# Kernel optimization log

Measured on AMD Instinct MI355X. Metric: run time of the kernel, lower is better.

## Reference

```python
import jax, jax.numpy as jnp
import numpy as np

VOCAB, FDIM = 100000, 256
N_NODES, N_UNIQUE, NUM_SAMPLE = 4096, 16384, 10
NEG = -9.0e15


def setup_inputs() -> dict:
    key = jax.random.key(0)
    k0, k1, k2, k3 = jax.random.split(key, 4)
    features = jax.random.normal(k0, (VOCAB, FDIM), dtype=jnp.float32)
    nodes = jax.random.randint(k1, (N_NODES,), 0, VOCAB, dtype=jnp.int64 if jax.config.jax_enable_x64 else jnp.int32)
    unique_ids = jax.random.randint(k2, (N_UNIQUE,), 0, VOCAB, dtype=nodes.dtype)
    neigh_idx = jax.random.randint(k3, (N_NODES, NUM_SAMPLE), 0, N_UNIQUE, dtype=nodes.dtype)
    return {"features": features, "nodes": nodes, "unique_ids": unique_ids, "neigh_idx": neigh_idx}


def reference(features, nodes, unique_ids, neigh_idx):
    # features: [V, F] lookup table (the `features` callable of the module)
    # nodes: [N] batch node ids; unique_ids: [M] unique sampled-neighbor ids
    # neigh_idx: [N, S] columns (into unique_ids) of each node's sampled neighbors
    N, _ = neigh_idx.shape
    M = unique_ids.shape[0]
    feature_matrix = features[nodes]        # [N, F]
    embed_matrix = features[unique_ids]     # [M, F]
    # binary adjacency mask built from (row, col) index pairs
    rows = jnp.arange(N)[:, None]           # [N, 1]
    mask = jnp.zeros((N, M), dtype=jnp.float32).at[rows, neigh_idx].set(1.0)
    scores = feature_matrix @ embed_matrix.T            # [N, M]
    scores = jnp.where(mask > 0, scores, NEG)           # masked with -9e15
    attention = jax.nn.softmax(scores, axis=1)          # softmax over dim=1
    to_feats = attention @ embed_matrix                 # [N, F]
    return to_feats
```

## Files before the change

### kernel.cpp

```cpp
#include <hip/hip_runtime.h>

#define FDIM 256
#define HALF 128
#define NSAMP 10
#define NEGF -9.0e15f


__global__ __launch_bounds__(256, 8) void AttentionAggregator_42477226557515_kernel(
    const float* __restrict__ features,
    const int* __restrict__ nodes_w,
    const int* __restrict__ uids_w,
    const int* __restrict__ nidx_w,
    float* __restrict__ out,
    int n_nodes)
{
    __shared__ float part[4][16];

    const int lane = threadIdx.x & 63;
    const int wid  = threadIdx.x >> 6;
    const int half = wid & 1;
    int n = (blockIdx.x << 1) + (wid >> 1);
    const bool live = (n < n_nodes);
    if (!live) n = 0;

    const unsigned long long oddnz = __ballot(nodes_w[2 * lane + 1] != 0);
    const bool i64 = (oddnz == 0ULL);

    const int off = half * HALF + (lane << 1);

    const int node_id = i64 ? nodes_w[2 * n] : nodes_w[n];
    const float2 sr = *(const float2*)(features + (size_t)node_id * FDIM + off);

    int c_own = 0;
    if (lane < NSAMP) {
        const int j = n * NSAMP + lane;
        c_own = i64 ? nidx_w[2 * j] : nidx_w[j];
    }
    int u_own = 0;
    if (lane < NSAMP)
        u_own = i64 ? uids_w[2 * c_own] : uids_w[c_own];

    bool vown = true;
#pragma unroll
    for (int t = 0; t < NSAMP; ++t) {
        const int ct = __shfl(c_own, t, 64);
        if (t < lane && ct == c_own) vown = false;
    }

    float2 e[NSAMP];
#pragma unroll
    for (int s = 0; s < NSAMP; ++s) {
        const int u = __shfl(u_own, s, 64);
        e[s] = *(const float2*)(features + (size_t)u * FDIM + off);
    }

    float part_own = 0.0f;
#pragma unroll
    for (int s = 0; s < NSAMP; ++s) {
        float p = sr.x * e[s].x + sr.y * e[s].y;
#pragma unroll
        for (int d = 32; d > 0; d >>= 1) p += __shfl_xor(p, d, 64);
        if (lane == s) part_own = p;
    }

    if (lane < NSAMP) part[wid][lane] = part_own;
    __syncthreads();
    const int partner = wid ^ 1;
    float sc_own = NEGF;
    if (lane < NSAMP && vown)
        sc_own = part[wid][lane] + part[partner][lane];

    float m = sc_own;
#pragma unroll
    for (int d = 32; d > 0; d >>= 1) m = fmaxf(m, __shfl_xor(m, d, 64));
    float w_own = (lane < NSAMP && vown) ? __expf(sc_own - m) : 0.0f;
    float l = w_own;
#pragma unroll
    for (int d = 32; d > 0; d >>= 1) l += __shfl_xor(l, d, 64);
    const float inv = 1.0f / l;

    float a0 = 0.0f, a1 = 0.0f;
#pragma unroll
    for (int s = 0; s < NSAMP; ++s) {
        const float ws = __shfl(w_own, s, 64);
        a0 += ws * e[s].x;
        a1 += ws * e[s].y;
    }

    if (live) {
        float2 o;
        o.x = a0 * inv;
        o.y = a1 * inv;
        *(float2*)(out + (size_t)n * FDIM + off) = o;
    }
}

extern "C" void kernel_launch(void* const* d_in, const int* in_sizes, int n_in,
                              void* d_out, int out_size, void* d_ws, size_t ws_size,
                              hipStream_t stream) {
    const float* features = (const float*)d_in[0];
    const int* nodes      = (const int*)d_in[1];
    const int* uids       = (const int*)d_in[2];
    const int* nidx       = (const int*)d_in[3];
    float* out            = (float*)d_out;

    const int n_nodes = out_size / FDIM;
    const int blocks  = (n_nodes + 1) / 2;

    hipLaunchKernelGGL(AttentionAggregator_42477226557515_kernel,
                       dim3(blocks), dim3(256), 0, stream,
                       features, nodes, uids, nidx, out, n_nodes);
}
```

Baseline: 143.0 us.

## Split neighbors across wave pair instead of feature halves, using float4 loads

Each node is still handled by two waves, but now each wave covers all 256 features for half of the 10 sampled neighbors instead of half the features for all neighbors. Full dot products are computed per wave, so the partial-score exchange is replaced by a shared score array. The weighted sums are combined through shared memory with a second barrier. This enables 16-byte float4 gathers and halves the shuffle reductions per wave, at the cost of an extra sync and an LDS round trip for the partial outputs.

```diff
diff --git a/kernel.cpp b/kernel.cpp
--- a/kernel.cpp
+++ b/kernel.cpp
@@ -1,8 +1,8 @@
 #include <hip/hip_runtime.h>
 
 #define FDIM 256
-#define HALF 128
 #define NSAMP 10
+#define HALFS 5
 #define NEGF -9.0e15f
 
 
@@ -14,22 +14,24 @@
     float* __restrict__ out,
     int n_nodes)
 {
-    __shared__ float part[4][16];
+    __shared__ float  sc_sm[2][16];
+    __shared__ float4 part[2][64];
 
     const int lane = threadIdx.x & 63;
     const int wid  = threadIdx.x >> 6;
-    const int half = wid & 1;
-    int n = (blockIdx.x << 1) + (wid >> 1);
+    const int nl   = wid >> 1;
+    const int h    = wid & 1;
+    int n = (blockIdx.x << 1) + nl;
     const bool live = (n < n_nodes);
     if (!live) n = 0;
 
     const unsigned long long oddnz = __ballot(nodes_w[2 * lane + 1] != 0);
     const bool i64 = (oddnz == 0ULL);
 
-    const int off = half * HALF + (lane << 1);
+    const int off = lane << 2;
 
     const int node_id = i64 ? nodes_w[2 * n] : nodes_w[n];
-    const float2 sr = *(const float2*)(features + (size_t)node_id * FDIM + off);
+    const float4 srv = *(const float4*)(features + (size_t)node_id * FDIM + off);
 
     int c_own = 0;
     if (lane < NSAMP) {
@@ -47,29 +49,27 @@
         if (t < lane && ct == c_own) vown = false;
     }
 
-    float2 e[NSAMP];
+    float4 e[HALFS];
 #pragma unroll
-    for (int s = 0; s < NSAMP; ++s) {
-        const int u = __shfl(u_own, s, 64);
-        e[s] = *(const float2*)(features + (size_t)u * FDIM + off);
+    for (int s = 0; s < HALFS; ++s) {
+        const int u = __shfl(u_own, h * HALFS + s, 64);
+        e[s] = *(const float4*)(features + (size_t)u * FDIM + off);
     }
 
-    float part_own = 0.0f;
+    float p_own = 0.0f;
 #pragma unroll
-    for (int s = 0; s < NSAMP; ++s) {
-        float p = sr.x * e[s].x + sr.y * e[s].y;
+    for (int s = 0; s < HALFS; ++s) {
+        float p = srv.x * e[s].x + srv.y * e[s].y + srv.z * e[s].z + srv.w * e[s].w;
 #pragma unroll
         for (int d = 32; d > 0; d >>= 1) p += __shfl_xor(p, d, 64);
-        if (lane == s) part_own = p;
+        if (lane == h * HALFS + s) p_own = p;
     }
+    if (lane >= h * HALFS && lane < (h + 1) * HALFS)
+        sc_sm[nl][lane] = p_own;
+    __syncthreads();
 
-    if (lane < NSAMP) part[wid][lane] = part_own;
-    __syncthreads();
-    const int partner = wid ^ 1;
     float sc_own = NEGF;
-    if (lane < NSAMP && vown)
-        sc_own = part[wid][lane] + part[partner][lane];
-
+    if (lane < NSAMP && vown) sc_own = sc_sm[nl][lane];
     float m = sc_own;
 #pragma unroll
     for (int d = 32; d > 0; d >>= 1) m = fmaxf(m, __shfl_xor(m, d, 64));
@@ -79,19 +79,29 @@
     for (int d = 32; d > 0; d >>= 1) l += __shfl_xor(l, d, 64);
     const float inv = 1.0f / l;
 
-    float a0 = 0.0f, a1 = 0.0f;
+    float a0 = 0.f, a1 = 0.f, a2 = 0.f, a3 = 0.f;
 #pragma unroll
-    for (int s = 0; s < NSAMP; ++s) {
-        const float ws = __shfl(w_own, s, 64);
+    for (int s = 0; s < HALFS; ++s) {
+        const float ws = __shfl(w_own, h * HALFS + s, 64);
         a0 += ws * e[s].x;
         a1 += ws * e[s].y;
+        a2 += ws * e[s].z;
+        a3 += ws * e[s].w;
     }
 
-    if (live) {
-        float2 o;
-        o.x = a0 * inv;
-        o.y = a1 * inv;
-        *(float2*)(out + (size_t)n * FDIM + off) = o;
+    if (h == 0) {
+        float4 pv; pv.x = a0; pv.y = a1; pv.z = a2; pv.w = a3;
+        part[nl][lane] = pv;
+    }
+    __syncthreads();
+    if (h == 1 && live) {
+        const float4 pv = part[nl][lane];
+        float4 o;
+        o.x = (a0 + pv.x) * inv;
+        o.y = (a1 + pv.y) * inv;
+        o.z = (a2 + pv.z) * inv;
+        o.w = (a3 + pv.w) * inv;
+        *(float4*)(out + (size_t)n * FDIM + off) = o;
     }
 }
 
```

Result: faster. 137.5 us (-3.8%).

## Map one wavefront per node with float4 gathers and a transposed butterfly reduction

Applied to the files above, without the earlier changes.

Each node is now handled by a single 64-lane wavefront loading float4 slices, instead of two wavefronts each covering half the feature row. This removes the shared-memory partial-sum exchange and the block barrier. The ten per-neighbor dot products are reduced with a transposed butterfly that splits the sums across lane halves, which needs fewer cross-lane shuffles than ten separate full reductions. Both int32 and int64 index interpretations are loaded up front so those loads are not serialized behind the width-detection ballot. In exchange, per-thread register use roughly doubles (float4 e[10]), and the launch-bounds occupancy hint is lowered to match.

```diff
diff --git a/kernel.cpp b/kernel.cpp
--- a/kernel.cpp
+++ b/kernel.cpp
@@ -1,12 +1,11 @@
 #include <hip/hip_runtime.h>
 
 #define FDIM 256
-#define HALF 128
 #define NSAMP 10
 #define NEGF -9.0e15f
 
 
-__global__ __launch_bounds__(256, 8) void AttentionAggregator_42477226557515_kernel(
+__global__ __launch_bounds__(256, 4) void AttentionAggregator_42477226557515_kernel(
     const float* __restrict__ features,
     const int* __restrict__ nodes_w,
     const int* __restrict__ uids_w,
@@ -14,28 +13,27 @@
     float* __restrict__ out,
     int n_nodes)
 {
-    __shared__ float part[4][16];
+    const int lane = threadIdx.x & 63;
+    const int n = (blockIdx.x << 2) + (threadIdx.x >> 6);
+    if (n >= n_nodes) return;
 
-    const int lane = threadIdx.x & 63;
-    const int wid  = threadIdx.x >> 6;
-    const int half = wid & 1;
-    int n = (blockIdx.x << 1) + (wid >> 1);
-    const bool live = (n < n_nodes);
-    if (!live) n = 0;
-
-    const unsigned long long oddnz = __ballot(nodes_w[2 * lane + 1] != 0);
-    const bool i64 = (oddnz == 0ULL);
-
-    const int off = half * HALF + (lane << 1);
-
-    const int node_id = i64 ? nodes_w[2 * n] : nodes_w[n];
-    const float2 sr = *(const float2*)(features + (size_t)node_id * FDIM + off);
-
-    int c_own = 0;
+    const int bw    = nodes_w[2 * lane + 1];
+    const int nid32 = nodes_w[n];
+    const int nid64 = nodes_w[2 * n];
+    int c32 = 0, c64 = 0;
     if (lane < NSAMP) {
         const int j = n * NSAMP + lane;
-        c_own = i64 ? nidx_w[2 * j] : nidx_w[j];
+        c32 = nidx_w[j];
+        c64 = nidx_w[2 * j];
     }
+    const unsigned long long oddnz = __ballot(bw != 0);
+    const bool i64 = (oddnz == 0ULL);
+    const int node_id = i64 ? nid64 : nid32;
+    const int c_own   = i64 ? c64 : c32;
+
+    const int off = lane << 2;
+
+    const float4 srv = *(const float4*)(features + (size_t)node_id * FDIM + off);
     int u_own = 0;
     if (lane < NSAMP)
         u_own = i64 ? uids_w[2 * c_own] : uids_w[c_own];
@@ -47,28 +45,53 @@
         if (t < lane && ct == c_own) vown = false;
     }
 
-    float2 e[NSAMP];
+    float4 e[NSAMP];
 #pragma unroll
     for (int s = 0; s < NSAMP; ++s) {
         const int u = __shfl(u_own, s, 64);
-        e[s] = *(const float2*)(features + (size_t)u * FDIM + off);
+        e[s] = *(const float4*)(features + (size_t)u * FDIM + off);
     }
 
-    float part_own = 0.0f;
+    float ps[NSAMP];
 #pragma unroll
-    for (int s = 0; s < NSAMP; ++s) {
-        float p = sr.x * e[s].x + sr.y * e[s].y;
+    for (int s = 0; s < NSAMP; ++s)
+        ps[s] = srv.x * e[s].x + srv.y * e[s].y + srv.z * e[s].z + srv.w * e[s].w;
+
+    const int b32 = (lane >> 5) & 1, b16 = (lane >> 4) & 1;
+    const int b8  = (lane >> 3) & 1, b4  = (lane >> 2) & 1;
+
+    float q[5];
 #pragma unroll
-        for (int d = 32; d > 0; d >>= 1) p += __shfl_xor(p, d, 64);
-        if (lane == s) part_own = p;
+    for (int i = 0; i < 5; ++i) {
+        const float keep = b32 ? ps[i + 5] : ps[i];
+        const float send = b32 ? ps[i] : ps[i + 5];
+        q[i] = keep + __shfl_xor(send, 32, 64);
     }
+    float r0, r1, r2;
+    { const float k = b16 ? q[3] : q[0], s_ = b16 ? q[0] : q[3]; r0 = k + __shfl_xor(s_, 16, 64); }
+    { const float k = b16 ? q[4] : q[1], s_ = b16 ? q[1] : q[4]; r1 = k + __shfl_xor(s_, 16, 64); }
+    r2 = q[2] + __shfl_xor(q[2], 16, 64);
+    float s0, s1;
+    { const float k = b8 ? r1 : r0, s_ = b8 ? r0 : r1; s0 = k + __shfl_xor(s_, 8, 64); }
+    s1 = r2 + __shfl_xor(r2, 8, 64);
+    float t0;
+    { const float k = b4 ? s1 : s0, s_ = b4 ? s0 : s1; t0 = k + __shfl_xor(s_, 4, 64); }
+    t0 += __shfl_xor(t0, 2, 64);
+    t0 += __shfl_xor(t0, 1, 64);
 
-    if (lane < NSAMP) part[wid][lane] = part_own;
-    __syncthreads();
-    const int partner = wid ^ 1;
-    float sc_own = NEGF;
-    if (lane < NSAMP && vown)
-        sc_own = part[wid][lane] + part[partner][lane];
+    int src;
+    {
+        const int bb32 = (lane >= 5) ? 1 : 0;
+        const int rr   = lane - 5 * bb32;
+        if (rr == 2) src = 4 + 32 * bb32;
+        else {
+            const int bb16 = (rr >= 3) ? 1 : 0;
+            const int bb8  = rr - 3 * bb16;
+            src = 8 * bb8 + 16 * bb16 + 32 * bb32;
+        }
+    }
+    const float sc_raw = __shfl(t0, src & 63, 64);
+    const float sc_own = (lane < NSAMP) ? sc_raw : NEGF;
 
     float m = sc_own;
 #pragma unroll
@@ -79,20 +102,19 @@
     for (int d = 32; d > 0; d >>= 1) l += __shfl_xor(l, d, 64);
     const float inv = 1.0f / l;
 
-    float a0 = 0.0f, a1 = 0.0f;
+    float a0 = 0.f, a1 = 0.f, a2 = 0.f, a3 = 0.f;
 #pragma unroll
     for (int s = 0; s < NSAMP; ++s) {
         const float ws = __shfl(w_own, s, 64);
         a0 += ws * e[s].x;
         a1 += ws * e[s].y;
+        a2 += ws * e[s].z;
+        a3 += ws * e[s].w;
     }
 
-    if (live) {
-        float2 o;
-        o.x = a0 * inv;
-        o.y = a1 * inv;
-        *(float2*)(out + (size_t)n * FDIM + off) = o;
-    }
+    float4 o;
+    o.x = a0 * inv; o.y = a1 * inv; o.z = a2 * inv; o.w = a3 * inv;
+    *(float4*)(out + (size_t)n * FDIM + off) = o;
 }
 
 extern "C" void kernel_launch(void* const* d_in, const int* in_sizes, int n_in,
@@ -105,7 +127,7 @@
     float* out            = (float*)d_out;
 
     const int n_nodes = out_size / FDIM;
-    const int blocks  = (n_nodes + 1) / 2;
+    const int blocks  = (n_nodes + 3) / 4;
 
     hipLaunchKernelGGL(AttentionAggregator_42477226557515_kernel,
                        dim3(blocks), dim3(256), 0, stream,
```

Measured after the change: 137.6 us. 3.8% less time.
